# Optimization experiments

Measured on AMD Instinct MI355X. Metric: run time of the kernel, lower is better.

## Reference

```python
import jax, jax.numpy as jnp
import numpy as np

NUM_HEADS = 8
NUM_POINTS = 4            # sampling points per pillar point
NUM_PILLAR = 4            # points in pillar
SAMPLING_RADIUS = 0.12


def masked_softmax(logits, mask):
    # logits/mask: [B, N, H, P]; softmax over last dim, robust to fully-masked rows
    m = mask.astype(logits.dtype)
    w = jax.nn.softmax(jnp.where(mask, logits, jnp.asarray(-1e9, logits.dtype)), axis=-1) * m
    return w / jnp.clip(jnp.sum(w, axis=-1, keepdims=True), 1e-6)


def grid_sample_bilinear(feat, loc):
    # feat: [G, D, H, W]; loc: [G, Nq, P, 2] normalized to [0,1]
    # matches torch grid_sample(mode='bilinear', padding_mode='zeros', align_corners=False)
    G, D, H, W = feat.shape
    _, Nq, P, _ = loc.shape
    fm = feat.reshape(G, D, H * W).transpose(0, 2, 1)  # [G, HW, D]
    x = loc[..., 0] * W - 0.5
    y = loc[..., 1] * H - 0.5
    x0 = jnp.floor(x)
    y0 = jnp.floor(y)
    wx = x - x0
    wy = y - y0
    out = jnp.zeros((G, Nq * P, D), dtype=feat.dtype)
    corners = [(0, 0, (1 - wx) * (1 - wy)), (1, 0, wx * (1 - wy)),
               (0, 1, (1 - wx) * wy), (1, 1, wx * wy)]
    for dx, dy, w in corners:
        xi = x0 + dx
        yi = y0 + dy
        valid = (xi >= 0) & (xi < W) & (yi >= 0) & (yi < H)
        xc = jnp.clip(xi, 0, W - 1).astype(jnp.int32)
        yc = jnp.clip(yi, 0, H - 1).astype(jnp.int32)
        idx = (yc * W + xc).reshape(G, Nq * P)
        g = jnp.take_along_axis(fm, idx[:, :, None], axis=1)  # [G, Nq*P, D]
        out = out + g * (w * valid.astype(feat.dtype)).reshape(G, Nq * P, 1)
    return out.reshape(G, Nq, P, D)


def setup_inputs() -> dict:
    key = jax.random.key(0)
    ks = jax.random.split(key, 10)
    B, N, C = 1, 10000, 256
    n_cams, Himg, Wimg = 6, 60, 100
    HD = NUM_HEADS * NUM_PILLAR * NUM_POINTS  # 128
    query = jax.random.normal(ks[0], (B, N, C), jnp.float32)
    image_feats = jax.random.normal(ks[1], (B, n_cams, C, Himg, Wimg), jnp.float32)
    reference_points_cam = jax.random.uniform(ks[2], (B, n_cams, N, NUM_PILLAR, 2), jnp.float32)
    bev_mask = jax.random.bernoulli(ks[3], 0.4, (B, n_cams, N, NUM_PILLAR))
    s = 0.02
    offset_W = jax.random.normal(ks[4], (C, HD * 2), jnp.float32) * s
    offset_b = jnp.zeros((HD * 2,), jnp.float32)
    weight_W = jax.random.normal(ks[5], (C, HD), jnp.float32) * s
    weight_b = jnp.zeros((HD,), jnp.float32)
    out_W = jax.random.normal(ks[6], (C, C), jnp.float32) * s
    out_b = jnp.zeros((C,), jnp.float32)
    return {"query": query, "image_feats": image_feats,
            "reference_points_cam": reference_points_cam, "bev_mask": bev_mask,
            "offset_W": offset_W, "offset_b": offset_b,
            "weight_W": weight_W, "weight_b": weight_b,
            "out_W": out_W, "out_b": out_b}


def reference(query, image_feats, reference_points_cam, bev_mask,
              offset_W, offset_b, weight_W, weight_b, out_W, out_b):
    B, N, C = query.shape
    _, n_cams, _, Himg, Wimg = image_feats.shape
    Hh, Pp, Pn = NUM_HEADS, NUM_PILLAR, NUM_POINTS
    P = Pp * Pn
    hd = C // Hh

    offsets = jnp.tanh(query @ offset_W + offset_b) * SAMPLING_RADIUS
    offsets = offsets.reshape(B, N, Hh, Pp, Pn, 2)
    weight_logits = (query @ weight_W + weight_b).reshape(B, N, Hh, P)

    fused = jnp.zeros((B, N, C), query.dtype)
    counts = jnp.zeros((B, N), jnp.int32)
    for cam in range(n_cams):
        ref = reference_points_cam[:, cam]          # [B, N, Pp, 2]
        visible = bev_mask[:, cam]                  # [B, N, Pp]
        loc = ref[:, :, None, :, None, :] + offsets  # [B, N, H, Pp, Pn, 2]
        loc = loc.reshape(B, N, Hh, P, 2)
        vmask = jnp.broadcast_to(visible[:, :, None, :, None], (B, N, Hh, Pp, Pn)).reshape(B, N, Hh, P)
        w = masked_softmax(weight_logits, vmask)    # [B, N, H, P]
        feat = image_feats[:, cam].reshape(B * Hh, hd, Himg, Wimg)
        grid = loc.transpose(0, 2, 1, 3, 4).reshape(B * Hh, N, P, 2)
        samp = grid_sample_bilinear(feat, grid)     # [B*H, N, P, hd]
        samp = samp.reshape(B, Hh, N, P, hd).transpose(0, 2, 1, 3, 4)  # [B, N, H, P, hd]
        cam_out = jnp.sum(samp * w[..., None], axis=3).reshape(B, N, C)
        has_vis = jnp.any(visible, axis=-1)         # [B, N]
        fused = fused + cam_out * has_vis[..., None].astype(cam_out.dtype)
        counts = counts + has_vis.astype(jnp.int32)
    fused = fused / jnp.clip(counts, 1)[..., None].astype(fused.dtype)
    return fused @ out_W + out_b
```

## Files before the change

### kernel.cpp

```cpp
#include <hip/hip_runtime.h>
#include <hip/hip_bf16.h>

#define N_Q   10000
#define N_CAM 6
#define HIMG  60
#define WIMG  100
#define NPIX  6000

typedef __attribute__((ext_vector_type(4))) float f32x4;
typedef __attribute__((ext_vector_type(2))) float f32x2;
typedef __attribute__((ext_vector_type(8))) short bf16x8;

__device__ __forceinline__ unsigned short f2bf(float x) {
  __hip_bfloat16 b = __float2bfloat16(x);
  return *reinterpret_cast<unsigned short*>(&b);
}
__device__ __forceinline__ float bf2f(unsigned short u) {
  return __uint_as_float(((unsigned)u) << 16);
}
__device__ __forceinline__ float bf16lo(unsigned int u) {
  return __uint_as_float(u << 16);
}
__device__ __forceinline__ void pk_fma(f32x2& acc, f32x2 a, f32x2 b) {
  asm("v_pk_fma_f32 %0, %1, %2, %0" : "+v"(acc) : "v"(a), "v"(b));
}

#define TRANS_BLKS (N_CAM * 94)
#define QVEC_BLKS  1250

__global__ __launch_bounds__(256) void prep_trans_k(
    const float* __restrict__ in,
    const float* __restrict__ q,
    const float* __restrict__ oW, const float* __restrict__ wW,
    const float* __restrict__ outW,
    unsigned short* __restrict__ ftout,
    unsigned short* __restrict__ qh,    unsigned short* __restrict__ ql,
    unsigned short* __restrict__ oWth,  unsigned short* __restrict__ oWtl,
    unsigned short* __restrict__ wWth,  unsigned short* __restrict__ wWtl,
    unsigned short* __restrict__ outWth,unsigned short* __restrict__ outWtl) {
  __shared__ float tile[64][65];
  const int tid = threadIdx.x;
  if (blockIdx.x < TRANS_BLKS) {
    const int cam = blockIdx.x / 94;
    const int px0 = (blockIdx.x % 94) * 64;
    const int lpx = tid & 63;
    const int cg  = tid >> 6;
    const int px  = px0 + lpx;
    const bool pv = px < NPIX;

    for (int c0 = 0; c0 < 256; c0 += 64) {
#pragma unroll
      for (int i = 0; i < 16; ++i) {
        int cc = cg * 16 + i;
        tile[lpx][cc] = pv ? in[(cam * 256 + c0 + cc) * NPIX + px] : 0.f;
      }
      __syncthreads();
      const int wc = tid & 63;
      const int pg = tid >> 6;
#pragma unroll
      for (int i = 0; i < 16; ++i) {
        int lp = pg * 16 + i;
        int gpx = px0 + lp;
        if (gpx < NPIX)
          ftout[(size_t)(cam * NPIX + gpx) * 256 + c0 + wc] = f2bf(tile[lp][wc]);
      }
      __syncthreads();
    }
    return;
  }
  if (blockIdx.x < TRANS_BLKS + QVEC_BLKS) {
    const int base = ((blockIdx.x - TRANS_BLKS) * 256 + tid) * 8;
    const float4 v0 = *reinterpret_cast<const float4*>(&q[base]);
    const float4 v1 = *reinterpret_cast<const float4*>(&q[base + 4]);
    float v[8] = {v0.x, v0.y, v0.z, v0.w, v1.x, v1.y, v1.z, v1.w};
    unsigned hw[4], lw[4];
#pragma unroll
    for (int j = 0; j < 4; ++j) {
      const unsigned short h0 = f2bf(v[2 * j]),  h1 = f2bf(v[2 * j + 1]);
      const unsigned short l0 = f2bf(v[2 * j] - bf2f(h0));
      const unsigned short l1 = f2bf(v[2 * j + 1] - bf2f(h1));
      hw[j] = (unsigned)h0 | ((unsigned)h1 << 16);
      lw[j] = (unsigned)l0 | ((unsigned)l1 << 16);
    }
    uint4 vh = {hw[0], hw[1], hw[2], hw[3]};
    uint4 vl = {lw[0], lw[1], lw[2], lw[3]};
    reinterpret_cast<uint4*>(qh)[base >> 3] = vh;
    reinterpret_cast<uint4*>(ql)[base >> 3] = vl;
    return;
  }
  const int b = blockIdx.x - TRANS_BLKS - QVEC_BLKS;
  const int k = tid;
  float v; unsigned short *dh, *dl; int idx;
  if (b < 256) {
    v = oW[k * 256 + b]; dh = oWth; dl = oWtl; idx = b * 256 + k;
  } else if (b < 384) {
    int nn = b - 256; v = wW[k * 128 + nn]; dh = wWth; dl = wWtl; idx = nn * 256 + k;
  } else {
    int nn = b - 384; v = outW[k * 256 + nn]; dh = outWth; dl = outWtl; idx = nn * 256 + k;
  }
  unsigned short hv = f2bf(v);
  dh[idx] = hv;
  dl[idx] = f2bf(v - bf2f(hv));
}

__device__ __forceinline__ void gemm_body(
    const unsigned short* __restrict__ Ah, const unsigned short* __restrict__ Al,
    const unsigned short* __restrict__ Bh, const unsigned short* __restrict__ Bl,
    const float* __restrict__ bias, float* __restrict__ C,
    int M, int N, int mode, int bm, int bn, int tid) {
  const int l = tid & 63, w = tid >> 6;
  const int wm = w >> 1, wn = w & 1;
  const int lr = l & 15;
  const int lk = (l >> 4) * 8;

  const int am0 = min(bm + wm * 32 + lr, M - 1);
  const int am1 = min(bm + wm * 32 + 16 + lr, M - 1);
  const int bn0 = bn + wn * 32 + lr;
  const int bn1 = bn0 + 16;

  const bf16x8* pah0 = (const bf16x8*)(Ah + (size_t)am0 * 256 + lk);
  const bf16x8* pah1 = (const bf16x8*)(Ah + (size_t)am1 * 256 + lk);
  const bf16x8* pal0 = (const bf16x8*)(Al + (size_t)am0 * 256 + lk);
  const bf16x8* pal1 = (const bf16x8*)(Al + (size_t)am1 * 256 + lk);
  const bf16x8* pbh0 = (const bf16x8*)(Bh + (size_t)bn0 * 256 + lk);
  const bf16x8* pbh1 = (const bf16x8*)(Bh + (size_t)bn1 * 256 + lk);
  const bf16x8* pbl0 = (const bf16x8*)(Bl + (size_t)bn0 * 256 + lk);
  const bf16x8* pbl1 = (const bf16x8*)(Bl + (size_t)bn1 * 256 + lk);

  f32x4 acc00 = {}, acc01 = {}, acc10 = {}, acc11 = {};

#pragma unroll
  for (int ks = 0; ks < 8; ++ks) {
    bf16x8 ah0 = pah0[ks * 4], ah1 = pah1[ks * 4];
    bf16x8 al0 = pal0[ks * 4], al1 = pal1[ks * 4];
    bf16x8 bh0 = pbh0[ks * 4], bh1 = pbh1[ks * 4];
    bf16x8 bl0 = pbl0[ks * 4], bl1 = pbl1[ks * 4];
    acc00 = __builtin_amdgcn_mfma_f32_16x16x32_bf16(ah0, bh0, acc00, 0, 0, 0);
    acc00 = __builtin_amdgcn_mfma_f32_16x16x32_bf16(ah0, bl0, acc00, 0, 0, 0);
    acc00 = __builtin_amdgcn_mfma_f32_16x16x32_bf16(al0, bh0, acc00, 0, 0, 0);
    acc01 = __builtin_amdgcn_mfma_f32_16x16x32_bf16(ah0, bh1, acc01, 0, 0, 0);
    acc01 = __builtin_amdgcn_mfma_f32_16x16x32_bf16(ah0, bl1, acc01, 0, 0, 0);
    acc01 = __builtin_amdgcn_mfma_f32_16x16x32_bf16(al0, bh1, acc01, 0, 0, 0);
    acc10 = __builtin_amdgcn_mfma_f32_16x16x32_bf16(ah1, bh0, acc10, 0, 0, 0);
    acc10 = __builtin_amdgcn_mfma_f32_16x16x32_bf16(ah1, bl0, acc10, 0, 0, 0);
    acc10 = __builtin_amdgcn_mfma_f32_16x16x32_bf16(al1, bh0, acc10, 0, 0, 0);
    acc11 = __builtin_amdgcn_mfma_f32_16x16x32_bf16(ah1, bh1, acc11, 0, 0, 0);
    acc11 = __builtin_amdgcn_mfma_f32_16x16x32_bf16(ah1, bl1, acc11, 0, 0, 0);
    acc11 = __builtin_amdgcn_mfma_f32_16x16x32_bf16(al1, bh1, acc11, 0, 0, 0);
  }

  const float bias0 = bias[bn + wn * 32 + lr];
  const float bias1 = bias[bn + wn * 32 + 16 + lr];
  const int row0 = bm + wm * 32 + (l >> 4) * 4;
  const int col0 = bn + wn * 32 + lr;
#pragma unroll
  for (int r = 0; r < 4; ++r) {
    int rowA = row0 + r, rowB = row0 + 16 + r;
    float v00 = acc00[r] + bias0, v01 = acc01[r] + bias1;
    float v10 = acc10[r] + bias0, v11 = acc11[r] + bias1;
    if (mode == 1) {
      v00 = tanhf(v00) * 0.12f; v01 = tanhf(v01) * 0.12f;
      v10 = tanhf(v10) * 0.12f; v11 = tanhf(v11) * 0.12f;
    } else if (mode == 2) {
      v00 = __expf(v00); v01 = __expf(v01);
      v10 = __expf(v10); v11 = __expf(v11);
    }
    if (rowA < M) {
      C[(size_t)rowA * N + col0] = v00;
      C[(size_t)rowA * N + col0 + 16] = v01;
    }
    if (rowB < M) {
      C[(size_t)rowB * N + col0] = v10;
      C[(size_t)rowB * N + col0 + 16] = v11;
    }
  }
}

__global__ __launch_bounds__(256) void gemm12_k(
    const unsigned short* __restrict__ Ah, const unsigned short* __restrict__ Al,
    const unsigned short* __restrict__ B1h, const unsigned short* __restrict__ B1l,
    const float* __restrict__ b1, float* __restrict__ C1,
    const unsigned short* __restrict__ B2h, const unsigned short* __restrict__ B2l,
    const float* __restrict__ b2, float* __restrict__ C2) {
  const int by = blockIdx.x;
  if (by < 4)
    gemm_body(Ah, Al, B1h, B1l, b1, C1, N_Q, 256, 1,
              blockIdx.y * 64, by * 64, threadIdx.x);
  else
    gemm_body(Ah, Al, B2h, B2l, b2, C2, N_Q, 128, 2,
              blockIdx.y * 64, (by - 4) * 64, threadIdx.x);
}

__global__ __launch_bounds__(256) void gemm_out_k(
    const unsigned short* __restrict__ Ah, const unsigned short* __restrict__ Al,
    const unsigned short* __restrict__ Bh, const unsigned short* __restrict__ Bl,
    const float* __restrict__ bias, float* __restrict__ C) {
  gemm_body(Ah, Al, Bh, Bl, bias, C, N_Q, 256, 0,
            blockIdx.y * 64, blockIdx.x * 64, threadIdx.x);
}

__global__ __launch_bounds__(256) void sample_cam(
    const unsigned short* __restrict__ ft,
    const float* __restrict__ offs,
    const float* __restrict__ wlog,
    const float* __restrict__ refp,
    const int*   __restrict__ mask,
    float* __restrict__ partial) {
  const int tid = threadIdx.x;
  const int sub = tid >> 7;
  const int t   = tid & 127;
  const int cam = blockIdx.x / (N_Q / 2);
  const int n   = (blockIdx.x % (N_Q / 2)) * 2 + sub;
  const int h   = t >> 4;
  const int p   = t & 15;
  const int pp  = p >> 2;
  const int c   = (t >> 2) & 3;
  const int ch  = t & 3;

  const int vis = mask[(cam * N_Q + n) * 4 + pp];
  const unsigned long long bal = __ballot(vis != 0);
  if (!(bal & 0x1111ULL)) return;

  __shared__ float spt[2][1216];
  float* lds = spt[sub];
  unsigned int* ldsu = reinterpret_cast<unsigned int*>(lds);

  const float2 off = reinterpret_cast<const float2*>(offs)[n * 128 + t];
  const float E = wlog[n * 128 + t];
  const uint4* ftq2 = reinterpret_cast<const uint4*>(ft)
                      + (size_t)cam * (NPIX * 32) + (unsigned)(h * 4 + ch);

  const int abase = h * 152 + p * 9;
  const int rbase = h * 152;

  float e = vis ? E : 0.f;
  float s = e;
#pragma unroll
  for (int m = 8; m >= 1; m >>= 1)
    s += __shfl_xor(s, m, 16);
  const float wgt = e / fmaxf(s, 1e-6f);

  const float2 ref = reinterpret_cast<const float2*>(refp)[(cam * N_Q + n) * 4 + pp];
  const float x = fmaf(ref.x + off.x, (float)WIMG, -0.5f);
  const float y = fmaf(ref.y + off.y, (float)HIMG, -0.5f);
  const float x0f = floorf(x), y0f = floorf(y);
  const float wx = x - x0f, wy = y - y0f;
  const int x0 = (int)x0f, y0 = (int)y0f;
  const int x1 = x0 + 1, y1 = y0 + 1;
  const float mx0 = (x0 >= 0 && x0 < WIMG) ? 1.f : 0.f;
  const float mx1 = (x1 >= 0 && x1 < WIMG) ? 1.f : 0.f;
  const float my0 = (y0 >= 0 && y0 < HIMG) ? 1.f : 0.f;
  const float my1 = (y1 >= 0 && y1 < HIMG) ? 1.f : 0.f;
  const int xc0 = min(max(x0, 0), WIMG - 1);
  const int xc1 = min(max(x1, 0), WIMG - 1);
  const int yc0 = min(max(y0, 0), HIMG - 1);
  const int yc1 = min(max(y1, 0), HIMG - 1);
  lds[abase + 0] = (1.f - wx) * (1.f - wy) * mx0 * my0 * wgt;
  lds[abase + 1] = wx * (1.f - wy) * mx1 * my0 * wgt;
  lds[abase + 2] = (1.f - wx) * wy * mx0 * my1 * wgt;
  lds[abase + 3] = wx * wy * mx1 * my1 * wgt;
  ldsu[abase + 4] = (unsigned)(yc0 * WIMG + xc0);
  ldsu[abase + 5] = (unsigned)(yc0 * WIMG + xc1);
  ldsu[abase + 6] = (unsigned)(yc1 * WIMG + xc0);
  ldsu[abase + 7] = (unsigned)(yc1 * WIMG + xc1);
  __builtin_amdgcn_wave_barrier();

  f32x2 acc2[4] = {{0.f, 0.f}, {0.f, 0.f}, {0.f, 0.f}, {0.f, 0.f}};
  const bool pv0 = (bal      ) & 1ULL;
  const bool pv1 = (bal >>  4) & 1ULL;
  const bool pv2 = (bal >>  8) & 1ULL;
  const bool pv3 = (bal >> 12) & 1ULL;
  uint4 u0[4], u1[4], u2[4], u3[4];

#define ISSUE(U, P)                                                          \
  if (pv##P) {                                                               \
    _Pragma("unroll")                                                        \
    for (int pn = 0; pn < 4; ++pn) {                                         \
      const unsigned pix = ldsu[rbase + ((P) * 4 + pn) * 9 + 4 + c];         \
      U[pn] = ftq2[pix * 32u];                                               \
    }                                                                        \
  }
  ISSUE(u0, 0) ISSUE(u1, 1) ISSUE(u2, 2) ISSUE(u3, 3)

#define CONSUME(U, P)                                                        \
  if (pv##P) {                                                               \
    _Pragma("unroll")                                                        \
    for (int pn = 0; pn < 4; ++pn) {                                         \
      const float wv = lds[rbase + ((P) * 4 + pn) * 9 + c];                  \
      const f32x2 w2 = {wv, wv};                                             \
      f32x2 a;                                                               \
      a.x = bf16lo(U[pn].x); a.y = __uint_as_float(U[pn].x);                 \
      pk_fma(acc2[0], a, w2);                                                \
      a.x = bf16lo(U[pn].y); a.y = __uint_as_float(U[pn].y);                 \
      pk_fma(acc2[1], a, w2);                                                \
      a.x = bf16lo(U[pn].z); a.y = __uint_as_float(U[pn].z);                 \
      pk_fma(acc2[2], a, w2);                                                \
      a.x = bf16lo(U[pn].w); a.y = __uint_as_float(U[pn].w);                 \
      pk_fma(acc2[3], a, w2);                                                \
    }                                                                        \
  }
  CONSUME(u0, 0) CONSUME(u1, 1) CONSUME(u2, 2) CONSUME(u3, 3)
#undef ISSUE
#undef CONSUME

  float acc[8];
#pragma unroll
  for (int j = 0; j < 4; ++j) { acc[2 * j] = acc2[j].x; acc[2 * j + 1] = acc2[j].y; }
#pragma unroll
  for (int j = 0; j < 8; ++j) acc[j] += __shfl_xor(acc[j], 4);
#pragma unroll
  for (int j = 0; j < 8; ++j) acc[j] += __shfl_xor(acc[j], 8);

  if (c == 0) {
    float* pb = partial + ((size_t)cam * N_Q + n) * 256 + h * 32 + ch * 8;
    f32x4 a0 = {acc[0], acc[1], acc[2], acc[3]};
    f32x4 a1 = {acc[4], acc[5], acc[6], acc[7]};
    *reinterpret_cast<f32x4*>(pb)     = a0;
    *reinterpret_cast<f32x4*>(pb + 4) = a1;
  }
}

__global__ __launch_bounds__(256) void combine_k(
    const float* __restrict__ partial,
    const int*   __restrict__ mask,
    unsigned short* __restrict__ fh,
    unsigned short* __restrict__ fl) {
  const int tid  = threadIdx.x;
  const int sub  = tid >> 6;
  const int lane = tid & 63;
  const int n    = blockIdx.x * 4 + sub;

  __shared__ int sv[4][6];
  if (tid < 24) {
    const int qi = tid / 6, cam = tid - qi * 6;
    const int nn = blockIdx.x * 4 + qi;
    const int4 m4 = *reinterpret_cast<const int4*>(&mask[(cam * N_Q + nn) * 4]);
    sv[qi][cam] = (m4.x | m4.y | m4.z | m4.w) ? 1 : 0;
  }
  __syncthreads();

  f32x4 s4 = {0.f, 0.f, 0.f, 0.f};
  int cnt = 0;
#pragma unroll
  for (int cam = 0; cam < N_CAM; ++cam) {
    if (sv[sub][cam]) {
      const f32x4 v = reinterpret_cast<const f32x4*>(partial)
                          [((size_t)cam * N_Q + n) * 64 + lane];
      s4 += v; cnt++;
    }
  }
  const float inv = (cnt > 0) ? (1.f / (float)cnt) : 1.f;
  unsigned short hs[4], ls[4];
#pragma unroll
  for (int j = 0; j < 4; ++j) {
    const float v = s4[j] * inv;
    hs[j] = f2bf(v);
    ls[j] = f2bf(v - bf2f(hs[j]));
  }
  uint2 vh = {(unsigned)hs[0] | ((unsigned)hs[1] << 16),
              (unsigned)hs[2] | ((unsigned)hs[3] << 16)};
  uint2 vl = {(unsigned)ls[0] | ((unsigned)ls[1] << 16),
              (unsigned)ls[2] | ((unsigned)ls[3] << 16)};
  reinterpret_cast<uint2*>(fh)[n * 64 + lane] = vh;
  reinterpret_cast<uint2*>(fl)[n * 64 + lane] = vl;
}

extern "C" void kernel_launch(void* const* d_in, const int* in_sizes, int n_in,
                              void* d_out, int out_size, void* d_ws, size_t ws_size,
                              hipStream_t stream) {
  const float* query = (const float*)d_in[0];
  const float* feats = (const float*)d_in[1];
  const float* refp  = (const float*)d_in[2];
  const int*   mask  = (const int*)d_in[3];
  const float* oW    = (const float*)d_in[4];
  const float* ob    = (const float*)d_in[5];
  const float* wW    = (const float*)d_in[6];
  const float* wb    = (const float*)d_in[7];
  const float* outW  = (const float*)d_in[8];
  const float* outb  = (const float*)d_in[9];
  float* out = (float*)d_out;

  char* wsb = (char*)d_ws;
  size_t o = 0;
  unsigned short* ft = (unsigned short*)(wsb + o); o += (size_t)N_CAM * NPIX * 256 * 2;
  unsigned short* qh = (unsigned short*)(wsb + o); o += (size_t)N_Q * 256 * 2;
  unsigned short* ql = (unsigned short*)(wsb + o); o += (size_t)N_Q * 256 * 2;
  unsigned short* fh = (unsigned short*)(wsb + o); o += (size_t)N_Q * 256 * 2;
  unsigned short* fl = (unsigned short*)(wsb + o); o += (size_t)N_Q * 256 * 2;
  unsigned short* oWth  = (unsigned short*)(wsb + o); o += 256 * 256 * 2;
  unsigned short* oWtl  = (unsigned short*)(wsb + o); o += 256 * 256 * 2;
  unsigned short* wWth  = (unsigned short*)(wsb + o); o += 128 * 256 * 2;
  unsigned short* wWtl  = (unsigned short*)(wsb + o); o += 128 * 256 * 2;
  unsigned short* outWth = (unsigned short*)(wsb + o); o += 256 * 256 * 2;
  unsigned short* outWtl = (unsigned short*)(wsb + o); o += 256 * 256 * 2;
  float* offs    = (float*)(wsb + o); o += (size_t)N_Q * 256 * 4;
  float* wlog    = (float*)(wsb + o); o += (size_t)N_Q * 128 * 4;
  float* partial = (float*)(wsb + o); o += (size_t)N_CAM * N_Q * 256 * 4;

  prep_trans_k<<<TRANS_BLKS + QVEC_BLKS + 640, 256, 0, stream>>>(
      feats, query, oW, wW, outW, ft, qh, ql,
      oWth, oWtl, wWth, wWtl, outWth, outWtl);

  dim3 g12(6, (N_Q + 63) / 64);
  gemm12_k<<<g12, 256, 0, stream>>>(qh, ql, oWth, oWtl, ob, offs,
                                    wWth, wWtl, wb, wlog);

  sample_cam<<<N_CAM * (N_Q / 2), 256, 0, stream>>>(ft, offs, wlog, refp, mask,
                                                    partial);

  combine_k<<<N_Q / 4, 256, 0, stream>>>(partial, mask, fh, fl);

  dim3 g3(4, (N_Q + 63) / 64);
  gemm_out_k<<<g3, 256, 0, stream>>>(fh, fl, outWth, outWtl, outb, out);
}
```

Before: 167.9 us.

## Loop sample_cam over several queries per block with prefetch; store bf16 partials

Each block now processes four query pairs in a loop instead of one. The per-query inputs (mask, offsets, logits, reference points) for the next iteration are prefetched while the current one is computed, and the LDS staging is double-buffered. The per-camera partial sums are written as bf16 rather than fp32, halving the partial buffer traffic between sample_cam and combine_k. The aim is to cut block launch overhead and memory traffic, at the cost of less parallelism across blocks and reduced precision in the intermediate partials.

```diff
diff --git a/kernel.cpp b/kernel.cpp
--- a/kernel.cpp
+++ b/kernel.cpp
@@ -20,6 +20,9 @@
 }
 __device__ __forceinline__ float bf16lo(unsigned int u) {
   return __uint_as_float(u << 16);
+}
+__device__ __forceinline__ float bf16hi(unsigned int u) {
+  return __uint_as_float(u & 0xffff0000u);
 }
 __device__ __forceinline__ void pk_fma(f32x2& acc, f32x2 a, f32x2 b) {
   asm("v_pk_fma_f32 %0, %1, %2, %0" : "+v"(acc) : "v"(a), "v"(b));
@@ -199,129 +202,152 @@
             blockIdx.y * 64, blockIdx.x * 64, threadIdx.x);
 }
 
+#define QPB   4
+#define QBLKS (N_Q / 2 / QPB)
+
 __global__ __launch_bounds__(256) void sample_cam(
     const unsigned short* __restrict__ ft,
     const float* __restrict__ offs,
     const float* __restrict__ wlog,
     const float* __restrict__ refp,
     const int*   __restrict__ mask,
-    float* __restrict__ partial) {
+    unsigned short* __restrict__ partial) {
   const int tid = threadIdx.x;
   const int sub = tid >> 7;
   const int t   = tid & 127;
-  const int cam = blockIdx.x / (N_Q / 2);
-  const int n   = (blockIdx.x % (N_Q / 2)) * 2 + sub;
+  const int cam = blockIdx.x / QBLKS;
+  const int q0  = (blockIdx.x % QBLKS) * QPB;
   const int h   = t >> 4;
   const int p   = t & 15;
   const int pp  = p >> 2;
   const int c   = (t >> 2) & 3;
   const int ch  = t & 3;
 
-  const int vis = mask[(cam * N_Q + n) * 4 + pp];
-  const unsigned long long bal = __ballot(vis != 0);
-  if (!(bal & 0x1111ULL)) return;
-
-  __shared__ float spt[2][1216];
-  float* lds = spt[sub];
-  unsigned int* ldsu = reinterpret_cast<unsigned int*>(lds);
-
-  const float2 off = reinterpret_cast<const float2*>(offs)[n * 128 + t];
-  const float E = wlog[n * 128 + t];
+  __shared__ float spt[2][2][1216];
+
   const uint4* ftq2 = reinterpret_cast<const uint4*>(ft)
                       + (size_t)cam * (NPIX * 32) + (unsigned)(h * 4 + ch);
 
-  const int abase = h * 152 + p * 9;
-  const int rbase = h * 152;
-
-  float e = vis ? E : 0.f;
-  float s = e;
-#pragma unroll
-  for (int m = 8; m >= 1; m >>= 1)
-    s += __shfl_xor(s, m, 16);
-  const float wgt = e / fmaxf(s, 1e-6f);
-
-  const float2 ref = reinterpret_cast<const float2*>(refp)[(cam * N_Q + n) * 4 + pp];
-  const float x = fmaf(ref.x + off.x, (float)WIMG, -0.5f);
-  const float y = fmaf(ref.y + off.y, (float)HIMG, -0.5f);
-  const float x0f = floorf(x), y0f = floorf(y);
-  const float wx = x - x0f, wy = y - y0f;
-  const int x0 = (int)x0f, y0 = (int)y0f;
-  const int x1 = x0 + 1, y1 = y0 + 1;
-  const float mx0 = (x0 >= 0 && x0 < WIMG) ? 1.f : 0.f;
-  const float mx1 = (x1 >= 0 && x1 < WIMG) ? 1.f : 0.f;
-  const float my0 = (y0 >= 0 && y0 < HIMG) ? 1.f : 0.f;
-  const float my1 = (y1 >= 0 && y1 < HIMG) ? 1.f : 0.f;
-  const int xc0 = min(max(x0, 0), WIMG - 1);
-  const int xc1 = min(max(x1, 0), WIMG - 1);
-  const int yc0 = min(max(y0, 0), HIMG - 1);
-  const int yc1 = min(max(y1, 0), HIMG - 1);
-  lds[abase + 0] = (1.f - wx) * (1.f - wy) * mx0 * my0 * wgt;
-  lds[abase + 1] = wx * (1.f - wy) * mx1 * my0 * wgt;
-  lds[abase + 2] = (1.f - wx) * wy * mx0 * my1 * wgt;
-  lds[abase + 3] = wx * wy * mx1 * my1 * wgt;
-  ldsu[abase + 4] = (unsigned)(yc0 * WIMG + xc0);
-  ldsu[abase + 5] = (unsigned)(yc0 * WIMG + xc1);
-  ldsu[abase + 6] = (unsigned)(yc1 * WIMG + xc0);
-  ldsu[abase + 7] = (unsigned)(yc1 * WIMG + xc1);
-  __builtin_amdgcn_wave_barrier();
-
-  f32x2 acc2[4] = {{0.f, 0.f}, {0.f, 0.f}, {0.f, 0.f}, {0.f, 0.f}};
-  const bool pv0 = (bal      ) & 1ULL;
-  const bool pv1 = (bal >>  4) & 1ULL;
-  const bool pv2 = (bal >>  8) & 1ULL;
-  const bool pv3 = (bal >> 12) & 1ULL;
-  uint4 u0[4], u1[4], u2[4], u3[4];
+  int n_pf = q0 * 2 + sub;
+  int    vis_n = mask[(cam * N_Q + n_pf) * 4 + pp];
+  float2 off_n = reinterpret_cast<const float2*>(offs)[n_pf * 128 + t];
+  float  E_n   = wlog[n_pf * 128 + t];
+  float2 ref_n = reinterpret_cast<const float2*>(refp)[(cam * N_Q + n_pf) * 4 + pp];
+
+  int buf = 0;
+  for (int it = 0; it < QPB; ++it) {
+    const int n = (q0 + it) * 2 + sub;
+    const int    vis = vis_n;
+    const float2 off = off_n;
+    const float  E   = E_n;
+    const float2 ref = ref_n;
+    const unsigned long long bal = __ballot(vis != 0);
+    if (it + 1 < QPB) {
+      const int n1 = (q0 + it + 1) * 2 + sub;
+      vis_n = mask[(cam * N_Q + n1) * 4 + pp];
+      off_n = reinterpret_cast<const float2*>(offs)[n1 * 128 + t];
+      E_n   = wlog[n1 * 128 + t];
+      ref_n = reinterpret_cast<const float2*>(refp)[(cam * N_Q + n1) * 4 + pp];
+    }
+    if (!(bal & 0x1111ULL)) continue;
+
+    float* lds = spt[buf][sub];
+    unsigned int* ldsu = reinterpret_cast<unsigned int*>(lds);
+    buf ^= 1;
+
+    const int abase = h * 152 + p * 9;
+    const int rbase = h * 152;
+
+    float e = vis ? E : 0.f;
+    float s = e;
+#pragma unroll
+    for (int m = 8; m >= 1; m >>= 1)
+      s += __shfl_xor(s, m, 16);
+    const float wgt = e / fmaxf(s, 1e-6f);
+
+    const float x = fmaf(ref.x + off.x, (float)WIMG, -0.5f);
+    const float y = fmaf(ref.y + off.y, (float)HIMG, -0.5f);
+    const float x0f = floorf(x), y0f = floorf(y);
+    const float wx = x - x0f, wy = y - y0f;
+    const int x0 = (int)x0f, y0 = (int)y0f;
+    const int x1 = x0 + 1, y1 = y0 + 1;
+    const float mx0 = (x0 >= 0 && x0 < WIMG) ? 1.f : 0.f;
+    const float mx1 = (x1 >= 0 && x1 < WIMG) ? 1.f : 0.f;
+    const float my0 = (y0 >= 0 && y0 < HIMG) ? 1.f : 0.f;
+    const float my1 = (y1 >= 0 && y1 < HIMG) ? 1.f : 0.f;
+    const int xc0 = min(max(x0, 0), WIMG - 1);
+    const int xc1 = min(max(x1, 0), WIMG - 1);
+    const int yc0 = min(max(y0, 0), HIMG - 1);
+    const int yc1 = min(max(y1, 0), HIMG - 1);
+    lds[abase + 0] = (1.f - wx) * (1.f - wy) * mx0 * my0 * wgt;
+    lds[abase + 1] = wx * (1.f - wy) * mx1 * my0 * wgt;
+    lds[abase + 2] = (1.f - wx) * wy * mx0 * my1 * wgt;
+    lds[abase + 3] = wx * wy * mx1 * my1 * wgt;
+    ldsu[abase + 4] = (unsigned)(yc0 * WIMG + xc0);
+    ldsu[abase + 5] = (unsigned)(yc0 * WIMG + xc1);
+    ldsu[abase + 6] = (unsigned)(yc1 * WIMG + xc0);
+    ldsu[abase + 7] = (unsigned)(yc1 * WIMG + xc1);
+    __builtin_amdgcn_wave_barrier();
+
+    f32x2 acc2[4] = {{0.f, 0.f}, {0.f, 0.f}, {0.f, 0.f}, {0.f, 0.f}};
+    const bool pv0 = (bal      ) & 1ULL;
+    const bool pv1 = (bal >>  4) & 1ULL;
+    const bool pv2 = (bal >>  8) & 1ULL;
+    const bool pv3 = (bal >> 12) & 1ULL;
+    uint4 u0[4], u1[4], u2[4], u3[4];
 
 #define ISSUE(U, P)                                                          \
-  if (pv##P) {                                                               \
-    _Pragma("unroll")                                                        \
-    for (int pn = 0; pn < 4; ++pn) {                                         \
-      const unsigned pix = ldsu[rbase + ((P) * 4 + pn) * 9 + 4 + c];         \
-      U[pn] = ftq2[pix * 32u];                                               \
-    }                                                                        \
-  }
-  ISSUE(u0, 0) ISSUE(u1, 1) ISSUE(u2, 2) ISSUE(u3, 3)
+    if (pv##P) {                                                             \
+      _Pragma("unroll")                                                      \
+      for (int pn = 0; pn < 4; ++pn) {                                       \
+        const unsigned pix = ldsu[rbase + ((P) * 4 + pn) * 9 + 4 + c];       \
+        U[pn] = ftq2[pix * 32u];                                             \
+      }                                                                      \
+    }
+    ISSUE(u0, 0) ISSUE(u1, 1) ISSUE(u2, 2) ISSUE(u3, 3)
 
 #define CONSUME(U, P)                                                        \
-  if (pv##P) {                                                               \
-    _Pragma("unroll")                                                        \
-    for (int pn = 0; pn < 4; ++pn) {                                         \
-      const float wv = lds[rbase + ((P) * 4 + pn) * 9 + c];                  \
-      const f32x2 w2 = {wv, wv};                                             \
-      f32x2 a;                                                               \
-      a.x = bf16lo(U[pn].x); a.y = __uint_as_float(U[pn].x);                 \
-      pk_fma(acc2[0], a, w2);                                                \
-      a.x = bf16lo(U[pn].y); a.y = __uint_as_float(U[pn].y);                 \
-      pk_fma(acc2[1], a, w2);                                                \
-      a.x = bf16lo(U[pn].z); a.y = __uint_as_float(U[pn].z);                 \
-      pk_fma(acc2[2], a, w2);                                                \
-      a.x = bf16lo(U[pn].w); a.y = __uint_as_float(U[pn].w);                 \
-      pk_fma(acc2[3], a, w2);                                                \
-    }                                                                        \
-  }
-  CONSUME(u0, 0) CONSUME(u1, 1) CONSUME(u2, 2) CONSUME(u3, 3)
+    if (pv##P) {                                                             \
+      _Pragma("unroll")                                                      \
+      for (int pn = 0; pn < 4; ++pn) {                                       \
+        const float wv = lds[rbase + ((P) * 4 + pn) * 9 + c];                \
+        const f32x2 w2 = {wv, wv};                                           \
+        f32x2 a;                                                             \
+        a.x = bf16lo(U[pn].x); a.y = __uint_as_float(U[pn].x);               \
+        pk_fma(acc2[0], a, w2);                                              \
+        a.x = bf16lo(U[pn].y); a.y = __uint_as_float(U[pn].y);               \
+        pk_fma(acc2[1], a, w2);                                              \
+        a.x = bf16lo(U[pn].z); a.y = __uint_as_float(U[pn].z);               \
+        pk_fma(acc2[2], a, w2);                                              \
+        a.x = bf16lo(U[pn].w); a.y = __uint_as_float(U[pn].w);               \
+        pk_fma(acc2[3], a, w2);                                              \
+      }                                                                      \
+    }
+    CONSUME(u0, 0) CONSUME(u1, 1) CONSUME(u2, 2) CONSUME(u3, 3)
 #undef ISSUE
 #undef CONSUME
 
-  float acc[8];
-#pragma unroll
-  for (int j = 0; j < 4; ++j) { acc[2 * j] = acc2[j].x; acc[2 * j + 1] = acc2[j].y; }
-#pragma unroll
-  for (int j = 0; j < 8; ++j) acc[j] += __shfl_xor(acc[j], 4);
-#pragma unroll
-  for (int j = 0; j < 8; ++j) acc[j] += __shfl_xor(acc[j], 8);
-
-  if (c == 0) {
-    float* pb = partial + ((size_t)cam * N_Q + n) * 256 + h * 32 + ch * 8;
-    f32x4 a0 = {acc[0], acc[1], acc[2], acc[3]};
-    f32x4 a1 = {acc[4], acc[5], acc[6], acc[7]};
-    *reinterpret_cast<f32x4*>(pb)     = a0;
-    *reinterpret_cast<f32x4*>(pb + 4) = a1;
+    float acc[8];
+#pragma unroll
+    for (int j = 0; j < 4; ++j) { acc[2 * j] = acc2[j].x; acc[2 * j + 1] = acc2[j].y; }
+#pragma unroll
+    for (int j = 0; j < 8; ++j) acc[j] += __shfl_xor(acc[j], 4);
+#pragma unroll
+    for (int j = 0; j < 8; ++j) acc[j] += __shfl_xor(acc[j], 8);
+
+    if (c == 0) {
+      unsigned w01 = (unsigned)f2bf(acc[0]) | ((unsigned)f2bf(acc[1]) << 16);
+      unsigned w23 = (unsigned)f2bf(acc[2]) | ((unsigned)f2bf(acc[3]) << 16);
+      unsigned w45 = (unsigned)f2bf(acc[4]) | ((unsigned)f2bf(acc[5]) << 16);
+      unsigned w67 = (unsigned)f2bf(acc[6]) | ((unsigned)f2bf(acc[7]) << 16);
+      uint4 v = {w01, w23, w45, w67};
+      reinterpret_cast<uint4*>(partial)[((size_t)cam * N_Q + n) * 32 + h * 4 + ch] = v;
+    }
   }
 }
 
 __global__ __launch_bounds__(256) void combine_k(
-    const float* __restrict__ partial,
+    const unsigned short* __restrict__ partial,
     const int*   __restrict__ mask,
     unsigned short* __restrict__ fh,
     unsigned short* __restrict__ fl) {
@@ -344,9 +370,11 @@
 #pragma unroll
   for (int cam = 0; cam < N_CAM; ++cam) {
     if (sv[sub][cam]) {
-      const f32x4 v = reinterpret_cast<const f32x4*>(partial)
+      const uint2 v = reinterpret_cast<const uint2*>(partial)
                           [((size_t)cam * N_Q + n) * 64 + lane];
-      s4 += v; cnt++;
+      s4[0] += bf16lo(v.x); s4[1] += bf16hi(v.x);
+      s4[2] += bf16lo(v.y); s4[3] += bf16hi(v.y);
+      cnt++;
     }
   }
   const float inv = (cnt > 0) ? (1.f / (float)cnt) : 1.f;
@@ -395,7 +423,8 @@
   unsigned short* outWtl = (unsigned short*)(wsb + o); o += 256 * 256 * 2;
   float* offs    = (float*)(wsb + o); o += (size_t)N_Q * 256 * 4;
   float* wlog    = (float*)(wsb + o); o += (size_t)N_Q * 128 * 4;
-  float* partial = (float*)(wsb + o); o += (size_t)N_CAM * N_Q * 256 * 4;
+  unsigned short* partial = (unsigned short*)(wsb + o);
+  o += (size_t)N_CAM * N_Q * 256 * 2;
 
   prep_trans_k<<<TRANS_BLKS + QVEC_BLKS + 640, 256, 0, stream>>>(
       feats, query, oW, wW, outW, ft, qh, ql,
@@ -405,8 +434,8 @@
   gemm12_k<<<g12, 256, 0, stream>>>(qh, ql, oWth, oWtl, ob, offs,
                                     wWth, wWtl, wb, wlog);
 
-  sample_cam<<<N_CAM * (N_Q / 2), 256, 0, stream>>>(ft, offs, wlog, refp, mask,
-                                                    partial);
+  sample_cam<<<N_CAM * QBLKS, 256, 0, stream>>>(ft, offs, wlog, refp, mask,
+                                                partial);
 
   combine_k<<<N_Q / 4, 256, 0, stream>>>(partial, mask, fh, fl);
 
```

After: 166.3 us. Within noise of the previous version (-0.9%).

## Fuse camera combine into output GEMM and store per-camera partials as bf16

Applied to the files above, without the earlier changes.

The separate combine kernel is removed. The output GEMM now builds its A operand by summing the visible cameras' partials directly, with visibility bits and the inverse count precomputed in the prep kernel. Per-camera partials are stored as bf16 instead of fp32, which halves the write and read traffic of the largest intermediate buffer and removes one launch plus the fh/fl round trip. In exchange the partials lose precision before averaging, and each of the 4 column blocks re-reads the partials.

```diff
diff --git a/kernel.cpp b/kernel.cpp
--- a/kernel.cpp
+++ b/kernel.cpp
@@ -21,23 +21,30 @@
 __device__ __forceinline__ float bf16lo(unsigned int u) {
   return __uint_as_float(u << 16);
 }
+__device__ __forceinline__ float bf16hi(unsigned int u) {
+  return __uint_as_float(u & 0xffff0000u);
+}
 __device__ __forceinline__ void pk_fma(f32x2& acc, f32x2 a, f32x2 b) {
   asm("v_pk_fma_f32 %0, %1, %2, %0" : "+v"(acc) : "v"(a), "v"(b));
 }
 
 #define TRANS_BLKS (N_CAM * 94)
 #define QVEC_BLKS  1250
+#define WT_BLKS    640
+#define VI_BLKS    40
 
 __global__ __launch_bounds__(256) void prep_trans_k(
     const float* __restrict__ in,
     const float* __restrict__ q,
     const float* __restrict__ oW, const float* __restrict__ wW,
     const float* __restrict__ outW,
+    const int*   __restrict__ mask,
     unsigned short* __restrict__ ftout,
     unsigned short* __restrict__ qh,    unsigned short* __restrict__ ql,
     unsigned short* __restrict__ oWth,  unsigned short* __restrict__ oWtl,
     unsigned short* __restrict__ wWth,  unsigned short* __restrict__ wWtl,
-    unsigned short* __restrict__ outWth,unsigned short* __restrict__ outWtl) {
+    unsigned short* __restrict__ outWth,unsigned short* __restrict__ outWtl,
+    uint2* __restrict__ vinfo) {
   __shared__ float tile[64][65];
   const int tid = threadIdx.x;
   if (blockIdx.x < TRANS_BLKS) {
@@ -88,19 +95,35 @@
     reinterpret_cast<uint4*>(ql)[base >> 3] = vl;
     return;
   }
-  const int b = blockIdx.x - TRANS_BLKS - QVEC_BLKS;
-  const int k = tid;
-  float v; unsigned short *dh, *dl; int idx;
-  if (b < 256) {
-    v = oW[k * 256 + b]; dh = oWth; dl = oWtl; idx = b * 256 + k;
-  } else if (b < 384) {
-    int nn = b - 256; v = wW[k * 128 + nn]; dh = wWth; dl = wWtl; idx = nn * 256 + k;
-  } else {
-    int nn = b - 384; v = outW[k * 256 + nn]; dh = outWth; dl = outWtl; idx = nn * 256 + k;
-  }
-  unsigned short hv = f2bf(v);
-  dh[idx] = hv;
-  dl[idx] = f2bf(v - bf2f(hv));
+  if (blockIdx.x < TRANS_BLKS + QVEC_BLKS + WT_BLKS) {
+    const int b = blockIdx.x - TRANS_BLKS - QVEC_BLKS;
+    const int k = tid;
+    float v; unsigned short *dh, *dl; int idx;
+    if (b < 256) {
+      v = oW[k * 256 + b]; dh = oWth; dl = oWtl; idx = b * 256 + k;
+    } else if (b < 384) {
+      int nn = b - 256; v = wW[k * 128 + nn]; dh = wWth; dl = wWtl; idx = nn * 256 + k;
+    } else {
+      int nn = b - 384; v = outW[k * 256 + nn]; dh = outWth; dl = outWtl; idx = nn * 256 + k;
+    }
+    unsigned short hv = f2bf(v);
+    dh[idx] = hv;
+    dl[idx] = f2bf(v - bf2f(hv));
+    return;
+  }
+  const int qq = (blockIdx.x - TRANS_BLKS - QVEC_BLKS - WT_BLKS) * 256 + tid;
+  if (qq < N_Q) {
+    unsigned bits = 0; int cnt = 0;
+#pragma unroll
+    for (int cam = 0; cam < N_CAM; ++cam) {
+      const int4 m4 = *reinterpret_cast<const int4*>(&mask[(cam * N_Q + qq) * 4]);
+      const int any = (m4.x | m4.y | m4.z | m4.w) ? 1 : 0;
+      bits |= (unsigned)any << cam;
+      cnt += any;
+    }
+    const float inv = (cnt > 0) ? (1.f / (float)cnt) : 1.f;
+    vinfo[qq] = make_uint2(bits, __float_as_uint(inv));
+  }
 }
 
 __device__ __forceinline__ void gemm_body(
@@ -192,11 +215,96 @@
 }
 
 __global__ __launch_bounds__(256) void gemm_out_k(
-    const unsigned short* __restrict__ Ah, const unsigned short* __restrict__ Al,
+    const unsigned short* __restrict__ partial,
+    const uint2* __restrict__ vinfo,
     const unsigned short* __restrict__ Bh, const unsigned short* __restrict__ Bl,
     const float* __restrict__ bias, float* __restrict__ C) {
-  gemm_body(Ah, Al, Bh, Bl, bias, C, N_Q, 256, 0,
-            blockIdx.y * 64, blockIdx.x * 64, threadIdx.x);
+  const int tid = threadIdx.x;
+  const int l = tid & 63, w = tid >> 6;
+  const int wm = w >> 1, wn = w & 1;
+  const int bm = blockIdx.y * 64, bn = blockIdx.x * 64;
+  const int lr = l & 15;
+  const int M = N_Q, N = 256;
+
+  const int am0 = min(bm + wm * 32 + lr, M - 1);
+  const int am1 = min(bm + wm * 32 + 16 + lr, M - 1);
+  const int bn0 = bn + wn * 32 + lr;
+  const int bn1 = bn0 + 16;
+
+  const uint2 vi0 = vinfo[am0], vi1 = vinfo[am1];
+  const float inv0 = __uint_as_float(vi0.y);
+  const float inv1 = __uint_as_float(vi1.y);
+  const uint4* pq = reinterpret_cast<const uint4*>(partial);
+
+  const int lk = (l >> 4) * 8;
+  const bf16x8* pbh0 = (const bf16x8*)(Bh + (size_t)bn0 * 256 + lk);
+  const bf16x8* pbh1 = (const bf16x8*)(Bh + (size_t)bn1 * 256 + lk);
+  const bf16x8* pbl0 = (const bf16x8*)(Bl + (size_t)bn0 * 256 + lk);
+  const bf16x8* pbl1 = (const bf16x8*)(Bl + (size_t)bn1 * 256 + lk);
+
+  f32x4 acc00 = {}, acc01 = {}, acc10 = {}, acc11 = {};
+
+#define BUILD_A(AH, AL, AM, BITS, INV)                                        \
+  {                                                                           \
+    float v[8] = {0.f, 0.f, 0.f, 0.f, 0.f, 0.f, 0.f, 0.f};                   \
+    _Pragma("unroll")                                                         \
+    for (int cam = 0; cam < N_CAM; ++cam) {                                   \
+      if ((BITS >> cam) & 1u) {                                               \
+        const uint4 u = pq[((size_t)cam * N_Q + (AM)) * 32 + slot];           \
+        v[0] += bf16lo(u.x); v[1] += bf16hi(u.x);                             \
+        v[2] += bf16lo(u.y); v[3] += bf16hi(u.y);                             \
+        v[4] += bf16lo(u.z); v[5] += bf16hi(u.z);                             \
+        v[6] += bf16lo(u.w); v[7] += bf16hi(u.w);                             \
+      }                                                                       \
+    }                                                                         \
+    _Pragma("unroll")                                                         \
+    for (int j = 0; j < 8; ++j) {                                             \
+      const float x = v[j] * (INV);                                           \
+      const unsigned short hb = f2bf(x);                                      \
+      AH[j] = (short)hb;                                                      \
+      AL[j] = (short)f2bf(x - bf2f(hb));                                      \
+    }                                                                         \
+  }
+
+#pragma unroll
+  for (int ks = 0; ks < 8; ++ks) {
+    const int slot = ks * 4 + (l >> 4);
+    bf16x8 ah0, al0, ah1, al1;
+    BUILD_A(ah0, al0, am0, vi0.x, inv0)
+    BUILD_A(ah1, al1, am1, vi1.x, inv1)
+    bf16x8 bh0 = pbh0[ks * 4], bh1 = pbh1[ks * 4];
+    bf16x8 bl0 = pbl0[ks * 4], bl1 = pbl1[ks * 4];
+    acc00 = __builtin_amdgcn_mfma_f32_16x16x32_bf16(ah0, bh0, acc00, 0, 0, 0);
+    acc00 = __builtin_amdgcn_mfma_f32_16x16x32_bf16(ah0, bl0, acc00, 0, 0, 0);
+    acc00 = __builtin_amdgcn_mfma_f32_16x16x32_bf16(al0, bh0, acc00, 0, 0, 0);
+    acc01 = __builtin_amdgcn_mfma_f32_16x16x32_bf16(ah0, bh1, acc01, 0, 0, 0);
+    acc01 = __builtin_amdgcn_mfma_f32_16x16x32_bf16(ah0, bl1, acc01, 0, 0, 0);
+    acc01 = __builtin_amdgcn_mfma_f32_16x16x32_bf16(al0, bh1, acc01, 0, 0, 0);
+    acc10 = __builtin_amdgcn_mfma_f32_16x16x32_bf16(ah1, bh0, acc10, 0, 0, 0);
+    acc10 = __builtin_amdgcn_mfma_f32_16x16x32_bf16(ah1, bl0, acc10, 0, 0, 0);
+    acc10 = __builtin_amdgcn_mfma_f32_16x16x32_bf16(al1, bh0, acc10, 0, 0, 0);
+    acc11 = __builtin_amdgcn_mfma_f32_16x16x32_bf16(ah1, bh1, acc11, 0, 0, 0);
+    acc11 = __builtin_amdgcn_mfma_f32_16x16x32_bf16(ah1, bl1, acc11, 0, 0, 0);
+    acc11 = __builtin_amdgcn_mfma_f32_16x16x32_bf16(al1, bh1, acc11, 0, 0, 0);
+  }
+#undef BUILD_A
+
+  const float bias0 = bias[bn + wn * 32 + lr];
+  const float bias1 = bias[bn + wn * 32 + 16 + lr];
+  const int row0 = bm + wm * 32 + (l >> 4) * 4;
+  const int col0 = bn + wn * 32 + lr;
+#pragma unroll
+  for (int r = 0; r < 4; ++r) {
+    int rowA = row0 + r, rowB = row0 + 16 + r;
+    if (rowA < M) {
+      C[(size_t)rowA * N + col0] = acc00[r] + bias0;
+      C[(size_t)rowA * N + col0 + 16] = acc01[r] + bias1;
+    }
+    if (rowB < M) {
+      C[(size_t)rowB * N + col0] = acc10[r] + bias0;
+      C[(size_t)rowB * N + col0 + 16] = acc11[r] + bias1;
+    }
+  }
 }
 
 __global__ __launch_bounds__(256) void sample_cam(
@@ -205,7 +313,7 @@
     const float* __restrict__ wlog,
     const float* __restrict__ refp,
     const int*   __restrict__ mask,
-    float* __restrict__ partial) {
+    unsigned short* __restrict__ partial) {
   const int tid = threadIdx.x;
   const int sub = tid >> 7;
   const int t   = tid & 127;
@@ -312,57 +420,13 @@
   for (int j = 0; j < 8; ++j) acc[j] += __shfl_xor(acc[j], 8);
 
   if (c == 0) {
-    float* pb = partial + ((size_t)cam * N_Q + n) * 256 + h * 32 + ch * 8;
-    f32x4 a0 = {acc[0], acc[1], acc[2], acc[3]};
-    f32x4 a1 = {acc[4], acc[5], acc[6], acc[7]};
-    *reinterpret_cast<f32x4*>(pb)     = a0;
-    *reinterpret_cast<f32x4*>(pb + 4) = a1;
-  }
-}
-
-__global__ __launch_bounds__(256) void combine_k(
-    const float* __restrict__ partial,
-    const int*   __restrict__ mask,
-    unsigned short* __restrict__ fh,
-    unsigned short* __restrict__ fl) {
-  const int tid  = threadIdx.x;
-  const int sub  = tid >> 6;
-  const int lane = tid & 63;
-  const int n    = blockIdx.x * 4 + sub;
-
-  __shared__ int sv[4][6];
-  if (tid < 24) {
-    const int qi = tid / 6, cam = tid - qi * 6;
-    const int nn = blockIdx.x * 4 + qi;
-    const int4 m4 = *reinterpret_cast<const int4*>(&mask[(cam * N_Q + nn) * 4]);
-    sv[qi][cam] = (m4.x | m4.y | m4.z | m4.w) ? 1 : 0;
-  }
-  __syncthreads();
-
-  f32x4 s4 = {0.f, 0.f, 0.f, 0.f};
-  int cnt = 0;
-#pragma unroll
-  for (int cam = 0; cam < N_CAM; ++cam) {
-    if (sv[sub][cam]) {
-      const f32x4 v = reinterpret_cast<const f32x4*>(partial)
-                          [((size_t)cam * N_Q + n) * 64 + lane];
-      s4 += v; cnt++;
-    }
-  }
-  const float inv = (cnt > 0) ? (1.f / (float)cnt) : 1.f;
-  unsigned short hs[4], ls[4];
-#pragma unroll
-  for (int j = 0; j < 4; ++j) {
-    const float v = s4[j] * inv;
-    hs[j] = f2bf(v);
-    ls[j] = f2bf(v - bf2f(hs[j]));
-  }
-  uint2 vh = {(unsigned)hs[0] | ((unsigned)hs[1] << 16),
-              (unsigned)hs[2] | ((unsigned)hs[3] << 16)};
-  uint2 vl = {(unsigned)ls[0] | ((unsigned)ls[1] << 16),
-              (unsigned)ls[2] | ((unsigned)ls[3] << 16)};
-  reinterpret_cast<uint2*>(fh)[n * 64 + lane] = vh;
-  reinterpret_cast<uint2*>(fl)[n * 64 + lane] = vl;
+    unsigned w01 = (unsigned)f2bf(acc[0]) | ((unsigned)f2bf(acc[1]) << 16);
+    unsigned w23 = (unsigned)f2bf(acc[2]) | ((unsigned)f2bf(acc[3]) << 16);
+    unsigned w45 = (unsigned)f2bf(acc[4]) | ((unsigned)f2bf(acc[5]) << 16);
+    unsigned w67 = (unsigned)f2bf(acc[6]) | ((unsigned)f2bf(acc[7]) << 16);
+    uint4 v = {w01, w23, w45, w67};
+    reinterpret_cast<uint4*>(partial)[((size_t)cam * N_Q + n) * 32 + h * 4 + ch] = v;
+  }
 }
 
 extern "C" void kernel_launch(void* const* d_in, const int* in_sizes, int n_in,
@@ -385,8 +449,6 @@
   unsigned short* ft = (unsigned short*)(wsb + o); o += (size_t)N_CAM * NPIX * 256 * 2;
   unsigned short* qh = (unsigned short*)(wsb + o); o += (size_t)N_Q * 256 * 2;
   unsigned short* ql = (unsigned short*)(wsb + o); o += (size_t)N_Q * 256 * 2;
-  unsigned short* fh = (unsigned short*)(wsb + o); o += (size_t)N_Q * 256 * 2;
-  unsigned short* fl = (unsigned short*)(wsb + o); o += (size_t)N_Q * 256 * 2;
   unsigned short* oWth  = (unsigned short*)(wsb + o); o += 256 * 256 * 2;
   unsigned short* oWtl  = (unsigned short*)(wsb + o); o += 256 * 256 * 2;
   unsigned short* wWth  = (unsigned short*)(wsb + o); o += 128 * 256 * 2;
@@ -395,11 +457,13 @@
   unsigned short* outWtl = (unsigned short*)(wsb + o); o += 256 * 256 * 2;
   float* offs    = (float*)(wsb + o); o += (size_t)N_Q * 256 * 4;
   float* wlog    = (float*)(wsb + o); o += (size_t)N_Q * 128 * 4;
-  float* partial = (float*)(wsb + o); o += (size_t)N_CAM * N_Q * 256 * 4;
-
-  prep_trans_k<<<TRANS_BLKS + QVEC_BLKS + 640, 256, 0, stream>>>(
-      feats, query, oW, wW, outW, ft, qh, ql,
-      oWth, oWtl, wWth, wWtl, outWth, outWtl);
+  unsigned short* partial = (unsigned short*)(wsb + o);
+  o += (size_t)N_CAM * N_Q * 256 * 2;
+  uint2* vinfo   = (uint2*)(wsb + o); o += (size_t)N_Q * 8;
+
+  prep_trans_k<<<TRANS_BLKS + QVEC_BLKS + WT_BLKS + VI_BLKS, 256, 0, stream>>>(
+      feats, query, oW, wW, outW, mask, ft, qh, ql,
+      oWth, oWtl, wWth, wWtl, outWth, outWtl, vinfo);
 
   dim3 g12(6, (N_Q + 63) / 64);
   gemm12_k<<<g12, 256, 0, stream>>>(qh, ql, oWth, oWtl, ob, offs,
@@ -408,8 +472,6 @@
   sample_cam<<<N_CAM * (N_Q / 2), 256, 0, stream>>>(ft, offs, wlog, refp, mask,
                                                     partial);
 
-  combine_k<<<N_Q / 4, 256, 0, stream>>>(partial, mask, fh, fl);
-
   dim3 g3(4, (N_Q + 63) / 64);
-  gemm_out_k<<<g3, 256, 0, stream>>>(fh, fl, outWth, outWtl, outb, out);
-}
+  gemm_out_k<<<g3, 256, 0, stream>>>(partial, vinfo, outWth, outWtl, outb, out);
+}
```

Result: slower. 175.4 us (+4.4%).
